# Optimization experiments

Measured on AMD Instinct MI355X. Metric: run time of the kernel, lower is better.

The kernel has to match this reference:

```python
import jax, jax.numpy as jnp
import numpy as np

B, N, D = 8, 1024, 768
H = 12
HD = D // H
LN_EPS = 1e-5
EPS = 1e-8


def setup_inputs() -> dict:
    key = jax.random.key(0)
    ks = jax.random.split(key, 16)
    s = 0.02
    return {
        "x": jax.random.normal(ks[0], (B, N, D), jnp.float32),
        "low_freq_feat": jax.random.normal(ks[1], (B, N, D), jnp.float32),
        "high_freq_feat": jax.random.normal(ks[2], (B, N, D), jnp.float32),
        "W_qkv_id": jax.random.normal(ks[3], (D, 3 * D), jnp.float32) * s,
        "W_qkv_attr": jax.random.normal(ks[4], (D, 3 * D), jnp.float32) * s,
        "W_fg_id": jax.random.normal(ks[5], (D, D), jnp.float32) * s,
        "b_fg_id": jnp.zeros((D,), jnp.float32),
        "W_fg_attr": jax.random.normal(ks[6], (D, D), jnp.float32) * s,
        "b_fg_attr": jnp.zeros((D,), jnp.float32),
        "W_proj_id": jax.random.normal(ks[7], (D, D), jnp.float32) * s,
        "b_proj_id": jnp.zeros((D,), jnp.float32),
        "W_proj_attr": jax.random.normal(ks[8], (D, D), jnp.float32) * s,
        "b_proj_attr": jnp.zeros((D,), jnp.float32),
        "ln_id_g": jnp.ones((D,), jnp.float32),
        "ln_id_b": jnp.zeros((D,), jnp.float32),
        "ln_attr_g": jnp.ones((D,), jnp.float32),
        "ln_attr_b": jnp.zeros((D,), jnp.float32),
        "ortho_temperature": jnp.float32(1.0),
        "freq_guide_strength": jnp.float32(0.3),
    }


def _layernorm(x, g, b):
    mu = x.mean(-1, keepdims=True)
    var = ((x - mu) ** 2).mean(-1, keepdims=True)
    return (x - mu) * jax.lax.rsqrt(var + LN_EPS) * g + b


def reference(x, low_freq_feat, high_freq_feat,
              W_qkv_id, W_qkv_attr,
              W_fg_id, b_fg_id, W_fg_attr, b_fg_attr,
              W_proj_id, b_proj_id, W_proj_attr, b_proj_attr,
              ln_id_g, ln_id_b, ln_attr_g, ln_attr_b,
              ortho_temperature, freq_guide_strength):
    b, n, d = x.shape
    scale = HD ** -0.5

    def split_qkv(t):
        t = t.reshape(b, n, 3, H, HD).transpose(2, 0, 3, 1, 4)
        return t[0], t[1], t[2]

    q_id, k_id, v_id = split_qkv(x @ W_qkv_id)
    q_at, k_at, v_at = split_qkv(x @ W_qkv_attr)

    fs = jax.nn.sigmoid(freq_guide_strength)
    low_g = (low_freq_feat @ W_fg_id + b_fg_id).reshape(b, n, H, HD).transpose(0, 2, 1, 3)
    high_g = (high_freq_feat @ W_fg_attr + b_fg_attr).reshape(b, n, H, HD).transpose(0, 2, 1, 3)
    v_id = v_id + fs * low_g
    v_at = v_at + fs * high_g

    def soft_attn(q, k):
        a = jnp.clip(jnp.einsum('bhnd,bhmd->bhnm', q, k) * scale, -20.0, 20.0)
        return jax.nn.softmax(a, axis=-1)

    attn_id = soft_attn(q_id, k_id)
    attn_at = soft_attn(q_at, k_at)

    # soft orthogonal mask (same mask for both branches)
    overlap = ((attn_id + EPS) * (attn_at + EPS)).sum(-1, keepdims=True)
    temp = jnp.clip(ortho_temperature, 0.1, 5.0)
    mask = jax.nn.sigmoid(-overlap * temp)

    def mask_renorm(a):
        m = a * mask
        m = m / (m.sum(-1, keepdims=True) + EPS)
        return jnp.where(jnp.isnan(m), jnp.zeros_like(m), m)

    attn_id = mask_renorm(attn_id)
    attn_at = mask_renorm(attn_at)

    def branch_out(a, v, W, bias, g, beta):
        o = jnp.einsum('bhnm,bhmd->bhnd', a, v).transpose(0, 2, 1, 3).reshape(b, n, d)
        return _layernorm(o @ W + bias, g, beta)

    id_features = branch_out(attn_id, v_id, W_proj_id, b_proj_id, ln_id_g, ln_id_b)
    attr_features = branch_out(attn_at, v_at, W_proj_attr, b_proj_attr, ln_attr_g, ln_attr_b)
    return (id_features, attr_features)
```

## Files before the change

kernel.cpp:

```cpp
#include <hip/hip_runtime.h>
#include <stdint.h>


typedef __attribute__((ext_vector_type(8))) _Float16 f16x8;
typedef __attribute__((ext_vector_type(4))) _Float16 f16x4;
typedef __attribute__((ext_vector_type(4))) float    f32x4;

__device__ __forceinline__ void g2l16(const void* g, void* l) {
  __builtin_amdgcn_global_load_lds(
      (const __attribute__((address_space(1))) void*)g,
      (__attribute__((address_space(3))) void*)l, 16, 0, 0);
}

#define BARX()   asm volatile("s_barrier" ::: "memory")
#define WAITV0() asm volatile("s_waitcnt vmcnt(0)" ::: "memory")
#define LGKM0()  asm volatile("s_waitcnt lgkmcnt(0)" ::: "memory")
#define SB0()    __builtin_amdgcn_sched_barrier(0)

#define MFMA12(NB)                                                            \
  __builtin_amdgcn_s_setprio(1);                                              \
  _Pragma("unroll")                                                           \
  for (int mt = 0; mt < 4; mt++)                                              \
    _Pragma("unroll")                                                         \
    for (int i = 0; i < 3; i++)                                               \
      acc[mt][(NB) + i] = SWAP                                                \
          ? __builtin_amdgcn_mfma_f32_16x16x32_f16(b[i], a[mt],               \
                                                   acc[mt][(NB) + i], 0, 0, 0)\
          : __builtin_amdgcn_mfma_f32_16x16x32_f16(a[mt], b[i],               \
                                                   acc[mt][(NB) + i], 0, 0, 0);\
  __builtin_amdgcn_s_setprio(0);

template <bool SWAP>
__device__ __forceinline__ void gemm192(const _Float16* __restrict__ A0,
                                        const _Float16* __restrict__ A1,
                                        const _Float16* __restrict__ B0,
                                        const _Float16* __restrict__ B1,
                                        int nb0, int nb1, int m0, int KT,
                                        _Float16* As, _Float16* Bs,
                                        f32x4 (&acc)[4][6]) {
  const int tid = threadIdx.x;
  const int lane = tid & 63, w = tid >> 6;
  const int wm = (w >> 1) * 64, wn = (w & 1) * 96;
  const int l15 = lane & 15, quad = lane >> 4;
  const int srow = lane >> 2;
  const int scol = ((lane & 3) ^ ((lane >> 3) & 3)) * 8;
  const int rg = (quad ^ ((l15 >> 1) & 3)) * 8;
  const int rdA = (wm + l15) * 32 + rg;
  const int rdB = (wn + l15) * 32 + rg;

  const _Float16* gA0a = A0 + (size_t)(m0 + (w * 2) * 16 + srow) * 768 + scol;
  const _Float16* gA1a = gA0a + (size_t)16 * 768;
  const _Float16* gA0b = A1 + (size_t)(m0 + (w * 2) * 16 + srow) * 768 + scol;
  const _Float16* gA1b = gA0b + (size_t)16 * 768;
  const _Float16* gBa[3]; const _Float16* gBb[3]; int lB[3];
#pragma unroll
  for (int i = 0; i < 3; i++) {
    int j = w * 3 + i, hb = j / 12, cb = j % 12;
    gBa[i] = B0 + (size_t)(nb0 + cb * 16 + srow) * 768 + hb * 32 + scol;
    gBb[i] = B1 + (size_t)(nb1 + cb * 16 + srow) * 768 + hb * 32 + scol;
    lB[i] = hb * 6144 + cb * 512;
  }

  auto stageA = [&](int t) {
    const bool s = t >= 12;
    const int kc = (s ? t - 12 : t) * 64;
    const _Float16* a0 = s ? gA0b : gA0a;
    const _Float16* a1 = s ? gA1b : gA1a;
    _Float16* Ab = As + (t & 1) * 16384 + w * 1024;
    g2l16(a0 + kc,      Ab);
    g2l16(a0 + kc + 32, Ab + 8192);
    g2l16(a1 + kc,      Ab + 512);
    g2l16(a1 + kc + 32, Ab + 8704);
  };
  auto stageB = [&](int t) {
    const bool s = t >= 12;
    const int kc = (s ? t - 12 : t) * 64;
    _Float16* Bb = Bs + (t & 1) * 12288;
#pragma unroll
    for (int i = 0; i < 3; i++) {
      const _Float16* p = s ? gBb[i] : gBa[i];
      g2l16(p + kc, Bb + lB[i]);
    }
  };

#pragma unroll
  for (int mt = 0; mt < 4; mt++)
#pragma unroll
    for (int nt = 0; nt < 6; nt++) acc[mt][nt] = (f32x4){0.f, 0.f, 0.f, 0.f};

  stageA(0); stageB(0);
  WAITV0();
  BARX();

  for (int t = 0; t < KT; t++) {
    const _Float16* as = As + (t & 1) * 16384;
    const _Float16* bs = Bs + (t & 1) * 12288;
    const bool st = (t + 1 < KT);
    f16x8 a[4], b[3];

#pragma unroll
    for (int mt = 0; mt < 4; mt++) a[mt] = *(const f16x8*)(as + rdA + mt * 512);
#pragma unroll
    for (int i = 0; i < 3; i++) b[i] = *(const f16x8*)(bs + rdB + i * 512);
    if (st) stageA(t + 1);
    BARX(); LGKM0(); SB0();
    MFMA12(0);
    SB0();
    BARX();

#pragma unroll
    for (int i = 0; i < 3; i++) b[i] = *(const f16x8*)(bs + rdB + (3 + i) * 512);
    if (st) stageB(t + 1);
    BARX(); LGKM0(); SB0();
    MFMA12(3);
    SB0();
    BARX();

#pragma unroll
    for (int mt = 0; mt < 4; mt++)
      a[mt] = *(const f16x8*)(as + 8192 + rdA + mt * 512);
#pragma unroll
    for (int i = 0; i < 3; i++)
      b[i] = *(const f16x8*)(bs + 6144 + rdB + i * 512);
    BARX(); LGKM0(); SB0();
    MFMA12(0);
    SB0();
    BARX();

#pragma unroll
    for (int i = 0; i < 3; i++)
      b[i] = *(const f16x8*)(bs + 6144 + rdB + (3 + i) * 512);
    BARX(); LGKM0(); SB0();
    MFMA12(3);
    SB0();
    WAITV0();
    BARX();
  }
}

__device__ __forceinline__ void tcast32(const float* __restrict__ src,
                                        _Float16* __restrict__ dst,
                                        int N, int n0, int k0) {
  __shared__ float t[32][33];
  int tr = threadIdx.x >> 5, tc = threadIdx.x & 31;
#pragma unroll
  for (int i = 0; i < 4; i++) {
    int r = tr + i * 8;
    t[r][tc] = src[(size_t)(k0 + r) * N + n0 + tc];
  }
  __syncthreads();
#pragma unroll
  for (int i = 0; i < 4; i++) {
    int r = tr + i * 8;
    dst[(size_t)(n0 + r) * 768 + k0 + tc] = (_Float16)t[tc][r];
  }
}

__global__ __launch_bounds__(256) void k_pre(const float* __restrict__ x,
                                             const float* __restrict__ lo,
                                             const float* __restrict__ hi,
                                             const float* __restrict__ fgs,
                                             const float* __restrict__ Wq0,
                                             const float* __restrict__ Wq1,
                                             const float* __restrict__ W0,
                                             const float* __restrict__ W1,
                                             const float* __restrict__ W2,
                                             const float* __restrict__ W3,
                                             _Float16* __restrict__ x_f,
                                             _Float16* __restrict__ low_f,
                                             _Float16* __restrict__ high_f,
                                             _Float16* __restrict__ Dq,
                                             _Float16* __restrict__ D0,
                                             _Float16* __restrict__ D1,
                                             _Float16* __restrict__ D2,
                                             _Float16* __restrict__ D3) {
  int blk = blockIdx.x;
  if (blk < 18432) {
    float scale = 1.f;
    const float* s; _Float16* d;
    if (blk < 6144)       { s = x;  d = x_f; }
    else if (blk < 12288) { s = lo; d = low_f;  blk -= 6144;
                            scale = 1.f / (1.f + __expf(-fgs[0])); }
    else                  { s = hi; d = high_f; blk -= 12288;
                            scale = 1.f / (1.f + __expf(-fgs[0])); }
    int i = blk * 256 + threadIdx.x;
    float4 v = ((const float4*)s)[i];
    f16x4 o = {(_Float16)(v.x * scale), (_Float16)(v.y * scale),
               (_Float16)(v.z * scale), (_Float16)(v.w * scale)};
    *(f16x4*)(d + (size_t)i * 4) = o;
    return;
  }
  blk -= 18432;
  if (blk < 3456) {
    int half = blk / 1728, rem = blk % 1728;
    int xx = rem % 72, yy = rem / 72;
    tcast32(half ? Wq1 : Wq0, Dq + (size_t)half * 2304 * 768, 2304, xx * 32, yy * 32);
  } else {
    blk -= 3456;
    int q = blk / 576, rem = blk % 576;
    int xx = rem % 24, yy = rem / 24;
    const float* src; _Float16* d;
    if (q == 0)      { src = W0; d = D0; }
    else if (q == 1) { src = W1; d = D1; }
    else if (q == 2) { src = W2; d = D2; }
    else             { src = W3; d = D3; }
    tcast32(src, d, 768, xx * 32, yy * 32);
  }
}

__global__ __launch_bounds__(512, 2) void k_gemm_qkv(const _Float16* __restrict__ x_f,
                                                     const _Float16* __restrict__ low_f,
                                                     const _Float16* __restrict__ high_f,
                                                     const _Float16* __restrict__ wqkvt,
                                                     const _Float16* __restrict__ wfgid,
                                                     const _Float16* __restrict__ wfgat,
                                                     const float* __restrict__ bfg_id,
                                                     const float* __restrict__ bfg_at,
                                                     const float* __restrict__ fgs,
                                                     _Float16* __restrict__ Qb,
                                                     _Float16* __restrict__ Kb,
                                                     _Float16* __restrict__ Vtb) {
  __shared__ alignas(16) _Float16 As[32768], Bs[24576];
  f32x4 acc[4][6];
  int bx = blockIdx.x, br = bx / 12, idx = bx % 12;
  int three = idx >> 2, sub = idx & 3;
  int m0 = blockIdx.y * 256;
  int n0abs = br * 2304 + three * 768 + sub * 192;
  int lane = threadIdx.x & 63, w = threadIdx.x >> 6;
  int wm = (w >> 1) * 64, wn = (w & 1) * 96, l15 = lane & 15, quad = lane >> 4;

  if (three == 2) {
    const _Float16* A1 = br ? high_f : low_f;
    const _Float16* B1 = br ? wfgat : wfgid;
    gemm192<false>(x_f, A1, wqkvt, B1, n0abs, sub * 192, m0, 24, As, Bs, acc);
    float fs = 1.f / (1.f + __expf(-fgs[0]));
    const float* bias = br ? bfg_at : bfg_id;
#pragma unroll
    for (int mt = 0; mt < 4; mt++)
#pragma unroll
      for (int nt = 0; nt < 6; nt++) {
        int c = sub * 192 + wn + nt * 16 + l15;
        int h = c >> 6, hd = c & 63;
        int m = m0 + wm + mt * 16 + quad * 4;
        int b = m >> 10, tok = m & 1023;
        size_t head = (size_t)(br * 96 + b * 12 + h);
        float bv = fs * bias[c];
        f32x4 v = acc[mt][nt];
        f16x4 o;
#pragma unroll
        for (int r = 0; r < 4; r++) o[r] = (_Float16)(v[r] + bv);
        *(f16x4*)(Vtb + (head * 64 + hd) * 1024 + tok) = o;
      }
  } else {
    gemm192<true>(x_f, x_f, wqkvt, wqkvt, n0abs, n0abs, m0, 12, As, Bs, acc);
    float qscl = (three == 0) ? 0.125f * 1.44269504f : 1.0f;
    _Float16* dst = (three == 0) ? Qb : Kb;
#pragma unroll
    for (int mt = 0; mt < 4; mt++)
#pragma unroll
      for (int nt = 0; nt < 6; nt++) {
        int m = m0 + wm + mt * 16 + l15;
        int c = sub * 192 + wn + nt * 16 + quad * 4;
        int h = c >> 6, hd = c & 63;
        int b = m >> 10, tok = m & 1023;
        size_t head = (size_t)(br * 96 + b * 12 + h);
        f32x4 v = acc[mt][nt];
        f16x4 o;
#pragma unroll
        for (int r = 0; r < 4; r++) o[r] = (_Float16)(v[r] * qscl);
        *(f16x4*)(dst + (head * 1024 + tok) * 64 + hd) = o;
      }
  }
}

__global__ __launch_bounds__(256, 3) void k_attn(const _Float16* __restrict__ Qb,
                                                 const _Float16* __restrict__ Kb,
                                                 const _Float16* __restrict__ Vtb,
                                                 _Float16* __restrict__ Ob) {
  __shared__ alignas(16) _Float16 Qs[128 * 64];
  __shared__ alignas(16) _Float16 Ks[128 * 64];
  __shared__ alignas(16) _Float16 Vts[64 * 128];
  int hl = blockIdx.x;
  int br = hl / 96, bh = hl % 96;
  int qbase = blockIdx.y * 128;
  const _Float16* Qh = Qb + (size_t)hl * 65536;
  const _Float16* Kh = Kb + (size_t)hl * 65536;
  const _Float16* Vth = Vtb + (size_t)hl * 65536;
  int lane = threadIdx.x & 63, w = threadIdx.x >> 6;
  int l15 = lane & 15, quad = lane >> 4;
  const int key7 = l15 & 7;

  {
    int rr = lane >> 3, sg = (lane & 7) ^ rr;
#pragma unroll
    for (int i = 0; i < 4; i++) {
      int c = w * 4 + i;
      g2l16(Qh + (size_t)(qbase + c * 8 + rr) * 64 + sg * 8, Qs + c * 512);
    }
  }
  auto stage_kv = [&](int n0) {
    int rr8 = lane >> 3, sg8 = ((lane & 7) ^ rr8) * 8;
    int rr16 = lane >> 4;
#pragma unroll
    for (int i = 0; i < 4; i++) {
      int c = w * 4 + i;
      g2l16(Kh + (size_t)(n0 + c * 8 + rr8) * 64 + sg8, Ks + c * 512);
      int vrow = c * 4 + rr16;
      int sg16 = ((lane & 15) ^ (vrow & 15)) * 8;
      g2l16(Vth + (size_t)vrow * 1024 + n0 + sg16, Vts + c * 512);
    }
  };
  stage_kv(0);

  f32x4 o[2][4];
#pragma unroll
  for (int qg = 0; qg < 2; qg++)
#pragma unroll
    for (int i = 0; i < 4; i++) o[qg][i] = (f32x4){0.f, 0.f, 0.f, 0.f};
  float rs0 = 0.f, rs1 = 0.f;
  f16x8 bq[2][2];
  const f32x4 zero = (f32x4){0.f, 0.f, 0.f, 0.f};
  const int g0 = (quad ^ key7) * 8, g1 = ((4 + quad) ^ key7) * 8;

  for (int kt = 0; kt < 8; kt++) {
    __syncthreads();
    if (kt == 0) {
#pragma unroll
      for (int qg = 0; qg < 2; qg++) {
        bq[qg][0] = *(const f16x8*)(Qs + (w * 32 + qg * 16 + l15) * 64 + g0);
        bq[qg][1] = *(const f16x8*)(Qs + (w * 32 + qg * 16 + l15) * 64 + g1);
      }
    }
    f32x4 c0, c1;
    {
      f16x8 a0 = *(const f16x8*)(Ks + l15 * 64 + g0);
      f16x8 a1 = *(const f16x8*)(Ks + l15 * 64 + g1);
      c0 = __builtin_amdgcn_mfma_f32_16x16x32_f16(a0, bq[0][0], zero, 0, 0, 0);
      c0 = __builtin_amdgcn_mfma_f32_16x16x32_f16(a1, bq[0][1], c0, 0, 0, 0);
      c1 = __builtin_amdgcn_mfma_f32_16x16x32_f16(a0, bq[1][0], zero, 0, 0, 0);
      c1 = __builtin_amdgcn_mfma_f32_16x16x32_f16(a1, bq[1][1], c1, 0, 0, 0);
    }
#pragma unroll
    for (int nt = 0; nt < 8; nt++) {
      f32x4 n0_, n1_;
      if (nt < 7) {
        f16x8 a0 = *(const f16x8*)(Ks + ((nt + 1) * 16 + l15) * 64 + g0);
        f16x8 a1 = *(const f16x8*)(Ks + ((nt + 1) * 16 + l15) * 64 + g1);
        n0_ = __builtin_amdgcn_mfma_f32_16x16x32_f16(a0, bq[0][0], zero, 0, 0, 0);
        n0_ = __builtin_amdgcn_mfma_f32_16x16x32_f16(a1, bq[0][1], n0_, 0, 0, 0);
        n1_ = __builtin_amdgcn_mfma_f32_16x16x32_f16(a0, bq[1][0], zero, 0, 0, 0);
        n1_ = __builtin_amdgcn_mfma_f32_16x16x32_f16(a1, bq[1][1], n1_, 0, 0, 0);
      }
      f16x4 pt0, pt1;
#pragma unroll
      for (int r = 0; r < 4; r++) {
        float p = __builtin_amdgcn_exp2f(c0[r]);
        rs0 += p; pt0[r] = (_Float16)p;
      }
#pragma unroll
      for (int r = 0; r < 4; r++) {
        float p = __builtin_amdgcn_exp2f(c1[r]);
        rs1 += p; pt1[r] = (_Float16)p;
      }
#pragma unroll
      for (int hdt = 0; hdt < 4; hdt++) {
        int g = ((2 * nt + (quad >> 1)) ^ l15) * 8 + (quad & 1) * 4;
        f16x4 av = *(const f16x4*)(Vts + (hdt * 16 + l15) * 128 + g);
        o[0][hdt] = __builtin_amdgcn_mfma_f32_16x16x16f16(av, pt0, o[0][hdt], 0, 0, 0);
        o[1][hdt] = __builtin_amdgcn_mfma_f32_16x16x16f16(av, pt1, o[1][hdt], 0, 0, 0);
      }
      if (nt < 7) { c0 = n0_; c1 = n1_; }
    }
    __syncthreads();
    if (kt < 7) stage_kv((kt + 1) * 128);
  }
  int b = bh / 12, h = bh % 12;
#pragma unroll
  for (int qg = 0; qg < 2; qg++) {
    float l = qg ? rs1 : rs0;
    l += __shfl_xor(l, 16);
    l += __shfl_xor(l, 32);
    float inv = 1.f / l;
    size_t rowb = ((size_t)br * 8192 + b * 1024 + qbase + w * 32 + qg * 16 + l15) * 768 +
                  h * 64;
#pragma unroll
    for (int hdt = 0; hdt < 4; hdt++) {
      f16x4 u;
#pragma unroll
      for (int r = 0; r < 4; r++) u[r] = (_Float16)(o[qg][hdt][r] * inv);
      *(f16x4*)(Ob + rowb + hdt * 16 + quad * 4) = u;
    }
  }
}

__global__ __launch_bounds__(512, 2) void k_gemm_proj2(const _Float16* __restrict__ Aid,
                                                       const _Float16* __restrict__ Aat,
                                                       const _Float16* __restrict__ Bid,
                                                       const _Float16* __restrict__ Bat,
                                                       _Float16* __restrict__ Yid,
                                                       _Float16* __restrict__ Yat) {
  __shared__ alignas(16) _Float16 As[32768], Bs[24576];
  f32x4 acc[4][6];
  int half = blockIdx.x >> 2;
  int n0 = (blockIdx.x & 3) * 192, m0 = blockIdx.y * 256;
  const _Float16* A = half ? Aat : Aid;
  const _Float16* Bt = half ? Bat : Bid;
  _Float16* Y = half ? Yat : Yid;
  gemm192<true>(A, A, Bt, Bt, n0, n0, m0, 12, As, Bs, acc);
  int lane = threadIdx.x & 63, w = threadIdx.x >> 6;
  int wm = (w >> 1) * 64, wn = (w & 1) * 96, l15 = lane & 15, quad = lane >> 4;
#pragma unroll
  for (int mt = 0; mt < 4; mt++)
#pragma unroll
    for (int nt = 0; nt < 6; nt++) {
      int m = m0 + wm + mt * 16 + l15;
      int n = n0 + wn + nt * 16 + quad * 4;
      f32x4 v = acc[mt][nt];
      f16x4 o;
#pragma unroll
      for (int r = 0; r < 4; r++) o[r] = (_Float16)v[r];
      *(f16x4*)(Y + (size_t)m * 768 + n) = o;
    }
}

__global__ __launch_bounds__(256) void k_ln(const _Float16* __restrict__ Yid,
                                            const _Float16* __restrict__ Yat,
                                            const float* __restrict__ bp_id,
                                            const float* __restrict__ bp_at,
                                            const float* __restrict__ g_id,
                                            const float* __restrict__ be_id,
                                            const float* __restrict__ g_at,
                                            const float* __restrict__ be_at,
                                            float* __restrict__ out) {
  int w = threadIdx.x >> 6, lane = threadIdx.x & 63;
  int r = blockIdx.x * 4 + w;
  int br = r >> 13, m = r & 8191;
  const _Float16* Y = br ? Yat : Yid;
  const float* bp = br ? bp_at : bp_id;
  const float* g = br ? g_at : g_id;
  const float* be = br ? be_at : be_id;
  float v[12], sum = 0.f, sq = 0.f;
#pragma unroll
  for (int j = 0; j < 3; j++) {
    int c = j * 256 + lane * 4;
    f16x4 y = *(const f16x4*)(Y + (size_t)m * 768 + c);
    float4 bv = *(const float4*)(bp + c);
#pragma unroll
    for (int r2 = 0; r2 < 4; r2++) {
      float t = (float)y[r2] + ((const float*)&bv)[r2];
      v[j * 4 + r2] = t; sum += t; sq += t * t;
    }
  }
#pragma unroll
  for (int d = 1; d < 64; d <<= 1) { sum += __shfl_xor(sum, d); sq += __shfl_xor(sq, d); }
  float mu = sum * (1.f / 768.f);
  float var = sq * (1.f / 768.f) - mu * mu;
  float rstd = rsqrtf(var + 1e-5f);
  float* op = out + (size_t)br * 6291456 + (size_t)m * 768;
#pragma unroll
  for (int j = 0; j < 3; j++) {
    int c = j * 256 + lane * 4;
    float4 gv = *(const float4*)(g + c);
    float4 bev = *(const float4*)(be + c);
    float4 ov;
#pragma unroll
    for (int r2 = 0; r2 < 4; r2++)
      ((float*)&ov)[r2] = (v[j * 4 + r2] - mu) * rstd * ((const float*)&gv)[r2] +
                          ((const float*)&bev)[r2];
    *(float4*)(op + c) = ov;
  }
}

extern "C" void kernel_launch(void* const* d_in, const int* in_sizes, int n_in,
                              void* d_out, int out_size, void* d_ws, size_t ws_size,
                              hipStream_t stream) {
  const float* x       = (const float*)d_in[0];
  const float* lowf    = (const float*)d_in[1];
  const float* highf   = (const float*)d_in[2];
  const float* Wqkv_id = (const float*)d_in[3];
  const float* Wqkv_at = (const float*)d_in[4];
  const float* Wfg_id  = (const float*)d_in[5];
  const float* bfg_id  = (const float*)d_in[6];
  const float* Wfg_at  = (const float*)d_in[7];
  const float* bfg_at  = (const float*)d_in[8];
  const float* Wpr_id  = (const float*)d_in[9];
  const float* bpr_id  = (const float*)d_in[10];
  const float* Wpr_at  = (const float*)d_in[11];
  const float* bpr_at  = (const float*)d_in[12];
  const float* g_id    = (const float*)d_in[13];
  const float* be_id   = (const float*)d_in[14];
  const float* g_at    = (const float*)d_in[15];
  const float* be_at   = (const float*)d_in[16];
  const float* fgs     = (const float*)d_in[18];

  char* ws = (char*)d_ws;
  _Float16* x_f    = (_Float16*)(ws + 0);
  _Float16* low_f  = (_Float16*)(ws + 12582912);
  _Float16* high_f = (_Float16*)(ws + 25165824);
  _Float16* wqkvt  = (_Float16*)(ws + 37748736);
  _Float16* wfgidt = (_Float16*)(ws + 44826624);
  _Float16* wfgatt = (_Float16*)(ws + 46006272);
  _Float16* wpridt = (_Float16*)(ws + 47185920);
  _Float16* wpratt = (_Float16*)(ws + 48365568);
  _Float16* Qb     = (_Float16*)(ws + 74711040);
  _Float16* Kb     = (_Float16*)(ws + 99876864);
  _Float16* Vtb    = (_Float16*)(ws + 125042688);
  _Float16* Ob     = (_Float16*)(ws + 150208512);
  _Float16* Y_id   = (_Float16*)(ws + 0);
  _Float16* Y_at   = (_Float16*)(ws + 49545216);

  k_pre<<<24192, 256, 0, stream>>>(x, lowf, highf, fgs,
                                   Wqkv_id, Wqkv_at, Wfg_id, Wfg_at, Wpr_id, Wpr_at,
                                   x_f, low_f, high_f,
                                   wqkvt, wfgidt, wfgatt, wpridt, wpratt);
  k_gemm_qkv<<<dim3(24, 32), 512, 0, stream>>>(x_f, low_f, high_f, wqkvt,
                                               wfgidt, wfgatt, bfg_id, bfg_at, fgs,
                                               Qb, Kb, Vtb);
  k_attn<<<dim3(192, 8), 256, 0, stream>>>(Qb, Kb, Vtb, Ob);
  k_gemm_proj2<<<dim3(8, 32), 512, 0, stream>>>(Ob, Ob + 6291456, wpridt, wpratt,
                                                Y_id, Y_at);
  k_ln<<<4096, 256, 0, stream>>>(Y_id, Y_at, bpr_id, bpr_at, g_id, be_id, g_at, be_at,
                                 (float*)d_out);
}
```

Measured before the change: 395.7 us.

## Prefetch next K/V tile into registers during attention compute; reorder QKV block mapping

```diff
diff --git a/kernel.cpp b/kernel.cpp
--- a/kernel.cpp
+++ b/kernel.cpp
@@ -10,6 +10,10 @@
   __builtin_amdgcn_global_load_lds(
       (const __attribute__((address_space(1))) void*)g,
       (__attribute__((address_space(3))) void*)l, 16, 0, 0);
+}
+
+__device__ __forceinline__ f16x8 gload8(const _Float16* p) {
+  return *(const __attribute__((address_space(1))) f16x8*)p;
 }
 
 #define BARX()   asm volatile("s_barrier" ::: "memory")
@@ -223,7 +227,8 @@
   __shared__ alignas(16) _Float16 As[32768], Bs[24576];
   f32x4 acc[4][6];
   int bx = blockIdx.x, br = bx / 12, idx = bx % 12;
-  int three = idx >> 2, sub = idx & 3;
+  int three = (idx < 4) ? 2 : ((idx < 8) ? 0 : 1);
+  int sub = idx & 3;
   int m0 = blockIdx.y * 256;
   int n0abs = br * 2304 + three * 768 + sub * 192;
   int lane = threadIdx.x & 63, w = threadIdx.x >> 6;
@@ -290,6 +295,19 @@
   int l15 = lane & 15, quad = lane >> 4;
   const int key7 = l15 & 7;
 
+  const int rr8 = lane >> 3, sg8 = ((lane & 7) ^ rr8) * 8;
+  const int rr16 = lane >> 4;
+  const _Float16* kSrc[4]; const _Float16* vSrc[4]; int dOff[4];
+#pragma unroll
+  for (int i = 0; i < 4; i++) {
+    int c = w * 4 + i;
+    kSrc[i] = Kh + (size_t)(c * 8 + rr8) * 64 + sg8;
+    int vrow = c * 4 + rr16;
+    int sg16 = ((lane & 15) ^ (vrow & 15)) * 8;
+    vSrc[i] = Vth + (size_t)vrow * 1024 + sg16;
+    dOff[i] = c * 512 + lane * 8;
+  }
+
   {
     int rr = lane >> 3, sg = (lane & 7) ^ rr;
 #pragma unroll
@@ -298,19 +316,20 @@
       g2l16(Qh + (size_t)(qbase + c * 8 + rr) * 64 + sg * 8, Qs + c * 512);
     }
   }
-  auto stage_kv = [&](int n0) {
-    int rr8 = lane >> 3, sg8 = ((lane & 7) ^ rr8) * 8;
-    int rr16 = lane >> 4;
-#pragma unroll
-    for (int i = 0; i < 4; i++) {
-      int c = w * 4 + i;
-      g2l16(Kh + (size_t)(n0 + c * 8 + rr8) * 64 + sg8, Ks + c * 512);
-      int vrow = c * 4 + rr16;
-      int sg16 = ((lane & 15) ^ (vrow & 15)) * 8;
-      g2l16(Vth + (size_t)vrow * 1024 + n0 + sg16, Vts + c * 512);
-    }
-  };
-  stage_kv(0);
+  f16x8 kreg[4], vreg[4];
+#pragma unroll
+  for (int i = 0; i < 4; i++) {
+    kreg[i] = gload8(kSrc[i]);
+    vreg[i] = gload8(vSrc[i]);
+  }
+  WAITV0();
+#pragma unroll
+  for (int i = 0; i < 4; i++) {
+    *(f16x8*)(Ks + dOff[i]) = kreg[i];
+    *(f16x8*)(Vts + dOff[i]) = vreg[i];
+  }
+  LGKM0();
+  BARX();
 
   f32x4 o[2][4];
 #pragma unroll
@@ -323,7 +342,15 @@
   const int g0 = (quad ^ key7) * 8, g1 = ((4 + quad) ^ key7) * 8;
 
   for (int kt = 0; kt < 8; kt++) {
-    __syncthreads();
+    if (kt < 7) {
+      int n0 = (kt + 1) * 128;
+#pragma unroll
+      for (int i = 0; i < 4; i++) {
+        kreg[i] = gload8(kSrc[i] + (size_t)n0 * 64);
+        vreg[i] = gload8(vSrc[i] + n0);
+      }
+      asm volatile("" ::: "memory");
+    }
     if (kt == 0) {
 #pragma unroll
       for (int qg = 0; qg < 2; qg++) {
@@ -371,8 +398,18 @@
       }
       if (nt < 7) { c0 = n0_; c1 = n1_; }
     }
-    __syncthreads();
-    if (kt < 7) stage_kv((kt + 1) * 128);
+    LGKM0();
+    BARX();
+    if (kt < 7) {
+      WAITV0();
+#pragma unroll
+      for (int i = 0; i < 4; i++) {
+        *(f16x8*)(Ks + dOff[i]) = kreg[i];
+        *(f16x8*)(Vts + dOff[i]) = vreg[i];
+      }
+      LGKM0();
+      BARX();
+    }
   }
   int b = bh / 12, h = bh % 12;
 #pragma unroll
```

Measured after the change: 466.8 us. 1.18x slower.
